# Optimization experiments

Measured on AMD Instinct MI355X. Metric: run time of the kernel, lower is better.

Reference implementation:

```python
import jax, jax.numpy as jnp
import numpy as np

B, LQ, D, DFF, NH, NL, NP = 16, 256, 256, 1024, 8, 4, 4
SHAPES = [(128, 128), (64, 64), (32, 32), (16, 16)]
S = sum(h * w for h, w in SHAPES)
DH = D // NH
OFFNORM = jnp.array([[w, h] for h, w in SHAPES], dtype=jnp.float32)  # (W,H) per level


def layer_norm(x, g, b, eps=1e-5):
    m = x.mean(-1, keepdims=True)
    v = jnp.mean((x - m) ** 2, axis=-1, keepdims=True)
    return (x - m) * jax.lax.rsqrt(v + eps) * g + b


def grid_sample_bilinear(img, grid):
    """img [N,C,H,W], grid [N,Hg,Wg,2] in [-1,1]; bilinear, zeros padding, align_corners=False."""
    N, C, H, W = img.shape
    Hg, Wg = grid.shape[1], grid.shape[2]
    x = (grid[..., 0] + 1.0) * (W * 0.5) - 0.5
    y = (grid[..., 1] + 1.0) * (H * 0.5) - 0.5
    x0 = jnp.floor(x); y0 = jnp.floor(y)
    wx1 = x - x0; wy1 = y - y0
    x0i = x0.astype(jnp.int32); y0i = y0.astype(jnp.int32)
    imgf = img.reshape(N, C, H * W)

    def tap(xi, yi, w):
        valid = (xi >= 0) & (xi < W) & (yi >= 0) & (yi < H)
        idx = (jnp.clip(yi, 0, H - 1) * W + jnp.clip(xi, 0, W - 1)).reshape(N, 1, Hg * Wg)
        return jnp.take_along_axis(imgf, idx, axis=2) * (w * valid).reshape(N, 1, Hg * Wg)

    out = (tap(x0i, y0i, (1 - wx1) * (1 - wy1)) + tap(x0i + 1, y0i, wx1 * (1 - wy1)) +
           tap(x0i, y0i + 1, (1 - wx1) * wy1) + tap(x0i + 1, y0i + 1, wx1 * wy1))
    return out.reshape(N, C, Hg, Wg)


def ms_sample(value, grids):
    """value [B,S,NH,DH], grids [B,Lq,NH,NL,NP,2] -> [B*NH, DH, Lq, NL*NP]."""
    Bv, Lq = value.shape[0], grids.shape[1]
    outs, start = [], 0
    for l, (h, w) in enumerate(SHAPES):
        v_l = value[:, start:start + h * w].transpose(0, 2, 3, 1).reshape(Bv * NH, DH, h, w)
        start += h * w
        g_l = grids[:, :, :, l].transpose(0, 2, 1, 3, 4).reshape(Bv * NH, Lq, NP, 2)
        outs.append(grid_sample_bilinear(v_l, g_l))  # [B*NH, DH, Lq, NP]
    return jnp.stack(outs, axis=3).reshape(Bv * NH, DH, Lq, NL * NP)


def mha(q, k, v, in_w, in_b, out_w, out_b, mask):
    d = q.shape[-1]
    Bq, Lq, Lk = q.shape[0], q.shape[1], k.shape[1]
    qh = (q @ in_w[:d].T + in_b[:d]).reshape(Bq, Lq, NH, DH).transpose(0, 2, 1, 3)
    kh = (k @ in_w[d:2 * d].T + in_b[d:2 * d]).reshape(Bq, Lk, NH, DH).transpose(0, 2, 1, 3)
    vh = (v @ in_w[2 * d:].T + in_b[2 * d:]).reshape(Bq, Lk, NH, DH).transpose(0, 2, 1, 3)
    logits = jnp.einsum('bhqd,bhkd->bhqk', qh, kh) * (DH ** -0.5) + mask
    o = jnp.einsum('bhqk,bhkd->bhqd', jax.nn.softmax(logits, axis=-1), vh)
    return o.transpose(0, 2, 1, 3).reshape(Bq, Lq, d) @ out_w.T + out_b


def _forward(tgt, query_pos, reference_points, src, tgt_masks,
             wq, wk, wv, so_w, so_b, sp_w, sp_b, aw_w, aw_b,
             sa_in_w, sa_in_b, sa_out_w, sa_out_b,
             ca_so_w, ca_so_b, ca_aw_w, ca_aw_b, ca_v_w, ca_v_b, ca_out_w, ca_out_b,
             l1_w, l1_b, l2_w, l2_b, n1_g, n1_b, n2_g, n2_b, n3_g, n3_b):
    # eval mode: dropout = identity; attn_concat_src=True; no kv cache.
    q = tgt @ wq.T + query_pos
    k = tgt @ wk.T
    v = tgt @ wv.T
    # ---- _sample_reference_points: grid_sample over levels, softmax over QUERY dim, sum over queries ----
    off = (tgt @ so_w.T + so_b).reshape(B, LQ, NH, NL, NP, 2)
    grids = 2.0 * (off / OFFNORM[None, None, None, :, None, :]) - 1.0
    aw = jax.nn.softmax((tgt @ aw_w.T + aw_b).reshape(B, LQ, NH, NL * NP), axis=1)
    value = (src @ sp_w.T + sp_b).reshape(B, S, NH, DH)
    sv = ms_sample(value, grids)                                       # [B*NH, DH, LQ, NL*NP]
    aw_r = aw.transpose(0, 2, 1, 3).reshape(B * NH, 1, LQ, NL * NP)
    sampled = (sv * aw_r).sum(axis=2).reshape(B, D, NL * NP).transpose(0, 2, 1)  # [B, NL*NP, D]
    # ---- self-attention with sampled src tokens prepended to k/v ----
    k = jnp.concatenate([sampled, k], axis=1)
    v = jnp.concatenate([sampled, v], axis=1)
    mask = jnp.concatenate([jnp.zeros((LQ, NL * NP), tgt.dtype), tgt_masks], axis=1)
    tgt = layer_norm(tgt + mha(q, k, v, sa_in_w, sa_in_b, sa_out_w, sa_out_b, mask), n2_g, n2_b)
    # ---- MSDeformAttn cross attention (2D reference points) ----
    qc = tgt + query_pos
    val2 = (src @ ca_v_w.T + ca_v_b).reshape(B, S, NH, DH)
    off2 = (qc @ ca_so_w.T + ca_so_b).reshape(B, LQ, NH, NL, NP, 2)
    aw2 = jax.nn.softmax((qc @ ca_aw_w.T + ca_aw_b).reshape(B, LQ, NH, NL * NP), axis=-1)
    loc2 = reference_points[:, :, None, :, None, :] + off2 / OFFNORM[None, None, None, :, None, :]
    sv2 = ms_sample(val2, 2.0 * loc2 - 1.0)                            # [B*NH, DH, LQ, NL*NP]
    out2 = (sv2 * aw2.transpose(0, 2, 1, 3).reshape(B * NH, 1, LQ, NL * NP)).sum(-1)
    out2 = out2.reshape(B, D, LQ).transpose(0, 2, 1) @ ca_out_w.T + ca_out_b
    tgt = layer_norm(tgt + out2, n1_g, n1_b)
    # ---- FFN ----
    ffn = jax.nn.relu(tgt @ l1_w.T + l1_b) @ l2_w.T + l2_b
    return layer_norm(tgt + ffn, n3_g, n3_b)


def setup_inputs():
    ks = iter(jax.random.split(jax.random.key(0), 48))
    rn = lambda s, sc=1.0: jax.random.normal(next(ks), s, dtype=jnp.float32) * sc
    W = 0.06  # ~1/sqrt(d_model)
    return dict(
        tgt=rn((B, LQ, D)),
        query_pos=rn((B, LQ, D)),
        reference_points=jax.random.uniform(next(ks), (B, LQ, NL, 2), dtype=jnp.float32),
        src=rn((B, S, D)),
        tgt_masks=jnp.zeros((LQ, LQ), jnp.float32),
        wq=rn((D, D), W), wk=rn((D, D), W), wv=rn((D, D), W),
        so_w=rn((NH * NL * NP * 2, D), 0.01),
        so_b=jax.random.uniform(next(ks), (NH * NL * NP * 2,), minval=-8.0, maxval=8.0),
        sp_w=rn((D, D), W), sp_b=rn((D,), W),
        aw_w=rn((NH * NL * NP, D), W), aw_b=rn((NH * NL * NP,), W),
        sa_in_w=rn((3 * D, D), W), sa_in_b=rn((3 * D,), W),
        sa_out_w=rn((D, D), W), sa_out_b=rn((D,), W),
        ca_so_w=rn((NH * NL * NP * 2, D), 0.01),
        ca_so_b=jax.random.uniform(next(ks), (NH * NL * NP * 2,), minval=-8.0, maxval=8.0),
        ca_aw_w=rn((NH * NL * NP, D), W), ca_aw_b=rn((NH * NL * NP,), W),
        ca_v_w=rn((D, D), W), ca_v_b=rn((D,), W),
        ca_out_w=rn((D, D), W), ca_out_b=rn((D,), W),
        l1_w=rn((DFF, D), W), l1_b=rn((DFF,), W),
        l2_w=rn((D, DFF), 0.03), l2_b=rn((D,), W),
        n1_g=jnp.ones((D,), jnp.float32), n1_b=jnp.zeros((D,), jnp.float32),
        n2_g=jnp.ones((D,), jnp.float32), n2_b=jnp.zeros((D,), jnp.float32),
        n3_g=jnp.ones((D,), jnp.float32), n3_b=jnp.zeros((D,), jnp.float32),
        src_spatial_shapes=jnp.array(SHAPES, jnp.int32),
        level_start_index=jnp.array(np.cumsum([0] + [h * w for h, w in SHAPES[:-1]]), jnp.int32),
    )


def reference(tgt, query_pos, reference_points, src, tgt_masks,
              wq, wk, wv, so_w, so_b, sp_w, sp_b, aw_w, aw_b,
              sa_in_w, sa_in_b, sa_out_w, sa_out_b,
              ca_so_w, ca_so_b, ca_aw_w, ca_aw_b, ca_v_w, ca_v_b, ca_out_w, ca_out_b,
              l1_w, l1_b, l2_w, l2_b, n1_g, n1_b, n2_g, n2_b, n3_g, n3_b,
              src_spatial_shapes, level_start_index):
    # src_spatial_shapes / level_start_index are static metadata (== SHAPES), baked in above.
    return _forward(tgt, query_pos, reference_points, src, tgt_masks,
                    wq, wk, wv, so_w, so_b, sp_w, sp_b, aw_w, aw_b,
                    sa_in_w, sa_in_b, sa_out_w, sa_out_b,
                    ca_so_w, ca_so_b, ca_aw_w, ca_aw_b, ca_v_w, ca_v_b, ca_out_w, ca_out_b,
                    l1_w, l1_b, l2_w, l2_b, n1_g, n1_b, n2_g, n2_b, n3_g, n3_b)
```

## Files before the change

### kernel.cpp

```cpp
#include <hip/hip_runtime.h>
#include <hip/hip_bf16.h>

#define NB   16
#define NLQ  256
#define ND   256
#define NDFF 1024
#define NNH  8
#define NNL  4
#define NNP  4
#define NDH  32
#define NS   21760
#define NLK  272

typedef __hip_bfloat16 bf16;
typedef unsigned short ushort_t;
typedef __bf16 bf16x8 __attribute__((ext_vector_type(8)));
typedef float f32x4 __attribute__((ext_vector_type(4)));
typedef unsigned short us4 __attribute__((ext_vector_type(4)));

__device__ __constant__ const int c_lvl_w[4]     = {128, 64, 32, 16};
__device__ __constant__ const int c_lvl_start[4] = {0, 16384, 20480, 21504};

__device__ __forceinline__ unsigned short f2bf(float x) {
  unsigned int u = __builtin_bit_cast(unsigned int, x);
  u += 0x7FFFu + ((u >> 16) & 1u);
  return (unsigned short)(u >> 16);
}

template<typename OT, bool RELU>
__global__ __launch_bounds__(256) void gemm_tn(const float* __restrict__ A,
                                               const float* __restrict__ W,
                                               const float* __restrict__ bias,
                                               const float* __restrict__ resid,
                                               OT* __restrict__ C,
                                               int M, int N, int K) {
  __shared__ float As[16][65];
  __shared__ float Ws[16][65];
  const int tid = threadIdx.x;
  const int tx = tid & 15, ty = tid >> 4;
  const int bn0 = blockIdx.x * 64, bm0 = blockIdx.y * 64;
  const int lr = tid >> 2;
  const int lk = (tid & 3) << 2;
  const float* Ap = A + (size_t)(bm0 + lr) * K + lk;
  const float* Wp = W + (size_t)(bn0 + lr) * K + lk;
  float acc[4][4] = {};
  for (int k0 = 0; k0 < K; k0 += 16) {
    float4 av = *(const float4*)(Ap + k0);
    float4 wv = *(const float4*)(Wp + k0);
    __syncthreads();
    As[lk + 0][lr] = av.x; As[lk + 1][lr] = av.y; As[lk + 2][lr] = av.z; As[lk + 3][lr] = av.w;
    Ws[lk + 0][lr] = wv.x; Ws[lk + 1][lr] = wv.y; Ws[lk + 2][lr] = wv.z; Ws[lk + 3][lr] = wv.w;
    __syncthreads();
#pragma unroll
    for (int k = 0; k < 16; ++k) {
      float a0 = As[k][ty * 4 + 0], a1 = As[k][ty * 4 + 1];
      float a2 = As[k][ty * 4 + 2], a3 = As[k][ty * 4 + 3];
      float b0 = Ws[k][tx * 4 + 0], b1 = Ws[k][tx * 4 + 1];
      float b2 = Ws[k][tx * 4 + 2], b3 = Ws[k][tx * 4 + 3];
      acc[0][0] += a0 * b0; acc[0][1] += a0 * b1; acc[0][2] += a0 * b2; acc[0][3] += a0 * b3;
      acc[1][0] += a1 * b0; acc[1][1] += a1 * b1; acc[1][2] += a1 * b2; acc[1][3] += a1 * b3;
      acc[2][0] += a2 * b0; acc[2][1] += a2 * b1; acc[2][2] += a2 * b2; acc[2][3] += a2 * b3;
      acc[3][0] += a3 * b0; acc[3][1] += a3 * b1; acc[3][2] += a3 * b2; acc[3][3] += a3 * b3;
    }
  }
#pragma unroll
  for (int i = 0; i < 4; ++i) {
    const int row = bm0 + ty * 4 + i;
#pragma unroll
    for (int j = 0; j < 4; ++j) {
      const int col = bn0 + tx * 4 + j;
      float c = acc[i][j];
      if (bias)  c += bias[col];
      if (resid) c += resid[(size_t)row * N + col];
      if (RELU)  c = fmaxf(c, 0.f);
      if constexpr (sizeof(OT) == 2) {
        C[(size_t)row * N + col] = __float2bfloat16(c);
      } else {
        C[(size_t)row * N + col] = c;
      }
    }
  }
}

__global__ __launch_bounds__(1024) void gemm_value_mfma(const float* __restrict__ A,
                                                        const ushort_t* __restrict__ Wb,
                                                        const float* __restrict__ bias,
                                                        ushort_t* __restrict__ C,
                                                        int M) {
  __shared__ __align__(16) ushort_t As[128][40];
  __shared__ __align__(16) ushort_t Bs[512][40];
  const int tid = threadIdx.x;
  const int wid = tid >> 6;
  const int lane = tid & 63;
  const int wm = wid >> 3;
  const int wn = wid & 7;
  const int bm0 = blockIdx.x * 128;
  const int lr = lane & 15;
  const int lk = (lane >> 4) * 8;

  const int ar = tid >> 3;
  const int ac4 = (tid & 7) * 4;
  const int br = tid >> 1;
  const int bc16 = (tid & 1) * 16;

  const float* Ap = A + (size_t)(bm0 + ar) * 256 + ac4;
  const ushort_t* Bp = Wb + (size_t)br * 256 + bc16;

  f32x4 acc[4][4] = {};

  for (int k0 = 0; k0 < 256; k0 += 32) {
    float4 av = *(const float4*)(Ap + k0);
    uint4 bv0 = *(const uint4*)(Bp + k0);
    uint4 bv1 = *(const uint4*)(Bp + k0 + 8);
    __syncthreads();
    us4 a4;
    a4[0] = f2bf(av.x); a4[1] = f2bf(av.y); a4[2] = f2bf(av.z); a4[3] = f2bf(av.w);
    *(us4*)&As[ar][ac4] = a4;
    *(uint4*)&Bs[br][bc16] = bv0;
    *(uint4*)&Bs[br][bc16 + 8] = bv1;
    __syncthreads();
    bf16x8 bfr[4];
#pragma unroll
    for (int ni = 0; ni < 4; ++ni)
      bfr[ni] = *(const bf16x8*)&Bs[wn * 64 + ni * 16 + lr][lk];
#pragma unroll
    for (int mi = 0; mi < 4; ++mi) {
      bf16x8 af = *(const bf16x8*)&As[wm * 64 + mi * 16 + lr][lk];
#pragma unroll
      for (int ni = 0; ni < 4; ++ni)
        acc[mi][ni] = __builtin_amdgcn_mfma_f32_16x16x32_bf16(af, bfr[ni], acc[mi][ni], 0, 0, 0);
    }
  }

  float bv[4];
#pragma unroll
  for (int ni = 0; ni < 4; ++ni) bv[ni] = bias[wn * 64 + ni * 16 + lr];
#pragma unroll
  for (int mi = 0; mi < 4; ++mi) {
#pragma unroll
    for (int r = 0; r < 4; ++r) {
      const int row = bm0 + wm * 64 + mi * 16 + (lane >> 4) * 4 + r;
#pragma unroll
      for (int ni = 0; ni < 4; ++ni) {
        const int col = wn * 64 + ni * 16 + lr;
        C[(size_t)row * 512 + col] = f2bf(acc[mi][ni][r] + bv[ni]);
      }
    }
  }
}

__global__ __launch_bounds__(256) void concat_w_kernel(const float* __restrict__ w1,
                                                       const float* __restrict__ w2,
                                                       const float* __restrict__ b1,
                                                       const float* __restrict__ b2,
                                                       ushort_t* __restrict__ wcat,
                                                       float* __restrict__ bcat) {
  int i = blockIdx.x * 256 + threadIdx.x;
  float v = (i < 65536) ? w1[i] : w2[i - 65536];
  wcat[i] = f2bf(v);
  if (i < 512) bcat[i] = (i < 256) ? b1[i] : b2[i - 256];
}

__global__ __launch_bounds__(64) void softmax_q_kernel(float* __restrict__ awl) {
  const int bc = blockIdx.x;
  const int c = bc & 127, b = bc >> 7;
  const int lane = threadIdx.x;
  float v[4];
  float mx = -1e30f;
#pragma unroll
  for (int i = 0; i < 4; ++i) {
    int q = lane + 64 * i;
    v[i] = awl[((size_t)(b * NLQ + q)) * 128 + c];
    mx = fmaxf(mx, v[i]);
  }
#pragma unroll
  for (int m = 32; m; m >>= 1) mx = fmaxf(mx, __shfl_xor(mx, m));
  float sum = 0.f;
#pragma unroll
  for (int i = 0; i < 4; ++i) { v[i] = __expf(v[i] - mx); sum += v[i]; }
#pragma unroll
  for (int m = 32; m; m >>= 1) sum += __shfl_xor(sum, m);
  float inv = 1.f / sum;
#pragma unroll
  for (int i = 0; i < 4; ++i) {
    int q = lane + 64 * i;
    awl[((size_t)(b * NLQ + q)) * 128 + c] = v[i] * inv;
  }
}

__global__ __launch_bounds__(128) void softmax16_kernel(float* __restrict__ aw2) {
  const int bq = blockIdx.x;
  const int c = threadIdx.x;
  float v = aw2[(size_t)bq * 128 + c];
  float mx = v;
#pragma unroll
  for (int m = 1; m < 16; m <<= 1) mx = fmaxf(mx, __shfl_xor(mx, m));
  float e = __expf(v - mx);
  float s = e;
#pragma unroll
  for (int m = 1; m < 16; m <<= 1) s += __shfl_xor(s, m);
  aw2[(size_t)bq * 128 + c] = e / s;
}

__global__ __launch_bounds__(256) void sample_sa_kernel(const bf16* __restrict__ vval,
                                                        const float* __restrict__ off1,
                                                        const float* __restrict__ aw,
                                                        float* __restrict__ sampled) {
  const int bid = blockIdx.x;
  const int lp = bid & 15, h = (bid >> 4) & 7, b = bid >> 7;
  const int l = lp >> 2, p = lp & 3;
  const int dh = threadIdx.x & 31, qg = threadIdx.x >> 5;
  const int Wd = c_lvl_w[l], st = c_lvl_start[l];
  const bf16* base = vval + ((size_t)b * NS + st) * 512 + h * 32 + dh;
  float acc = 0.f;
  for (int q = qg; q < NLQ; q += 8) {
    const float* op = off1 + (size_t)(b * NLQ + q) * 256 + ((h * 4 + l) * 4 + p) * 2;
    float x = op[0] - 0.5f;
    float y = op[1] - 0.5f;
    float w = aw[(size_t)(b * NLQ + q) * 128 + h * 16 + lp];
    float x0f = floorf(x), y0f = floorf(y);
    int x0 = (int)x0f, y0 = (int)y0f;
    float wx1 = x - x0f, wy1 = y - y0f;
    float wx0 = 1.f - wx1, wy0 = 1.f - wy1;
    auto tap = [&](int xi, int yi) -> float {
      if (xi < 0 || xi >= Wd || yi < 0 || yi >= Wd) return 0.f;
      return __bfloat162float(base[(size_t)(yi * Wd + xi) * 512]);
    };
    float v00 = tap(x0, y0),     v10 = tap(x0 + 1, y0);
    float v01 = tap(x0, y0 + 1), v11 = tap(x0 + 1, y0 + 1);
    acc += w * (wy0 * (wx0 * v00 + wx1 * v10) + wy1 * (wx0 * v01 + wx1 * v11));
  }
  __shared__ float red[8][32];
  red[qg][dh] = acc;
  __syncthreads();
  if (qg == 0) {
    float s = acc;
#pragma unroll
    for (int g = 1; g < 8; ++g) s += red[g][dh];
    sampled[((size_t)b * 16 + lp) * 256 + h * 32 + dh] = s;
  }
}

__global__ __launch_bounds__(256) void sample_ca_kernel(const bf16* __restrict__ vval,
                                                        const float* __restrict__ off2,
                                                        const float* __restrict__ aw2,
                                                        const float* __restrict__ refp,
                                                        float* __restrict__ out2) {
  const int bq = blockIdx.x;
  const int b = bq >> 8, q = bq & 255;
  const int h = threadIdx.x >> 5, dh = threadIdx.x & 31;
  float acc = 0.f;
#pragma unroll
  for (int lp = 0; lp < 16; ++lp) {
    const int l = lp >> 2, p = lp & 3;
    const int Wd = c_lvl_w[l], st = c_lvl_start[l];
    float rx = refp[((size_t)(b * NLQ + q) * 4 + l) * 2 + 0];
    float ry = refp[((size_t)(b * NLQ + q) * 4 + l) * 2 + 1];
    const float* op = off2 + (size_t)(b * NLQ + q) * 256 + ((h * 4 + l) * 4 + p) * 2;
    float x = rx * Wd + op[0] - 0.5f;
    float y = ry * Wd + op[1] - 0.5f;
    float w = aw2[(size_t)(b * NLQ + q) * 128 + h * 16 + lp];
    const bf16* base = vval + ((size_t)b * NS + st) * 512 + 256 + h * 32 + dh;
    float x0f = floorf(x), y0f = floorf(y);
    int x0 = (int)x0f, y0 = (int)y0f;
    float wx1 = x - x0f, wy1 = y - y0f;
    float wx0 = 1.f - wx1, wy0 = 1.f - wy1;
    auto tap = [&](int xi, int yi) -> float {
      if (xi < 0 || xi >= Wd || yi < 0 || yi >= Wd) return 0.f;
      return __bfloat162float(base[(size_t)(yi * Wd + xi) * 512]);
    };
    float v00 = tap(x0, y0),     v10 = tap(x0 + 1, y0);
    float v01 = tap(x0, y0 + 1), v11 = tap(x0 + 1, y0 + 1);
    acc += w * (wy0 * (wx0 * v00 + wx1 * v10) + wy1 * (wx0 * v01 + wx1 * v11));
  }
  out2[(size_t)(b * NLQ + q) * 256 + h * 32 + dh] = acc;
}

__global__ __launch_bounds__(256) void concat_kv_kernel(const float* __restrict__ sampled,
                                                        const float* __restrict__ kin,
                                                        const float* __restrict__ vin,
                                                        float* __restrict__ kcat,
                                                        float* __restrict__ vcat) {
  const int r = blockIdx.x;
  const int b = r / NLK, j = r % NLK;
  const int t = threadIdx.x;
  float kv, vv;
  if (j < 16) {
    kv = sampled[((size_t)b * 16 + j) * 256 + t];
    vv = kv;
  } else {
    kv = kin[((size_t)(b * NLQ + (j - 16))) * 256 + t];
    vv = vin[((size_t)(b * NLQ + (j - 16))) * 256 + t];
  }
  kcat[(size_t)r * 256 + t] = kv;
  vcat[(size_t)r * 256 + t] = vv;
}

__global__ __launch_bounds__(64) void attn_kernel(const float* __restrict__ qh,
                                                  const float* __restrict__ kh,
                                                  const float* __restrict__ vh,
                                                  const float* __restrict__ tmask,
                                                  float* __restrict__ attno) {
  const int bid = blockIdx.x;
  const int q = bid & 255, h = (bid >> 8) & 7, b = bid >> 11;
  const int lane = threadIdx.x;
  __shared__ float qrow[32];
  __shared__ float p[NLK];
  if (lane < 32) qrow[lane] = qh[((size_t)(b * NLQ + q)) * 256 + h * 32 + lane];
  __syncthreads();
  const float scale = 0.17677669529663687f;
  float s[5];
  float mx = -1e30f;
#pragma unroll
  for (int i = 0; i < 5; ++i) {
    int kk = lane + i * 64;
    float val = -1e30f;
    if (kk < NLK) {
      const float* kr = kh + ((size_t)(b * NLK + kk)) * 256 + h * 32;
      float d = 0.f;
#pragma unroll
      for (int c = 0; c < 32; ++c) d += qrow[c] * kr[c];
      val = d * scale;
      if (kk >= 16) val += tmask[(size_t)q * NLQ + (kk - 16)];
    }
    s[i] = val;
    mx = fmaxf(mx, val);
  }
#pragma unroll
  for (int m = 32; m; m >>= 1) mx = fmaxf(mx, __shfl_xor(mx, m));
  float sum = 0.f;
#pragma unroll
  for (int i = 0; i < 5; ++i) {
    int kk = lane + i * 64;
    if (kk < NLK) { s[i] = __expf(s[i] - mx); sum += s[i]; }
  }
#pragma unroll
  for (int m = 32; m; m >>= 1) sum += __shfl_xor(sum, m);
  const float inv = 1.f / sum;
#pragma unroll
  for (int i = 0; i < 5; ++i) {
    int kk = lane + i * 64;
    if (kk < NLK) p[kk] = s[i] * inv;
  }
  __syncthreads();
  if (lane < 32) {
    float acc = 0.f;
    const float* vb = vh + ((size_t)b * NLK) * 256 + h * 32 + lane;
    for (int kk = 0; kk < NLK; ++kk) acc += p[kk] * vb[(size_t)kk * 256];
    attno[((size_t)(b * NLQ + q)) * 256 + h * 32 + lane] = acc;
  }
}

__global__ __launch_bounds__(256) void add_ln_kernel(const float* __restrict__ resid,
                                                     const float* __restrict__ x,
                                                     const float* __restrict__ g,
                                                     const float* __restrict__ bt,
                                                     float* __restrict__ out) {
  const int row = blockIdx.x;
  const int t = threadIdx.x;
  const size_t idx = (size_t)row * 256 + t;
  float v = resid[idx] + x[idx];
  __shared__ float red[4];
  float s = v;
#pragma unroll
  for (int m = 32; m; m >>= 1) s += __shfl_xor(s, m);
  const int wid = t >> 6;
  if ((t & 63) == 0) red[wid] = s;
  __syncthreads();
  float mean = (red[0] + red[1] + red[2] + red[3]) * (1.f / 256.f);
  float d = v - mean;
  float s2 = d * d;
#pragma unroll
  for (int m = 32; m; m >>= 1) s2 += __shfl_xor(s2, m);
  __syncthreads();
  if ((t & 63) == 0) red[wid] = s2;
  __syncthreads();
  float var = (red[0] + red[1] + red[2] + red[3]) * (1.f / 256.f);
  out[idx] = d * rsqrtf(var + 1e-5f) * g[t] + bt[t];
}

__global__ __launch_bounds__(256) void add_kernel(const float* __restrict__ a,
                                                  const float* __restrict__ b,
                                                  float* __restrict__ c, int n) {
  int i = blockIdx.x * 256 + threadIdx.x;
  if (i < n) c[i] = a[i] + b[i];
}


static inline void gemm_f32(hipStream_t s, const float* A, const float* W,
                            const float* bias, const float* resid, float* C,
                            int M, int N, int K, bool relu = false) {
  dim3 g(N / 64, M / 64);
  if (relu) gemm_tn<float, true><<<g, 256, 0, s>>>(A, W, bias, resid, C, M, N, K);
  else      gemm_tn<float, false><<<g, 256, 0, s>>>(A, W, bias, resid, C, M, N, K);
}

extern "C" void kernel_launch(void* const* d_in, const int* in_sizes, int n_in,
                              void* d_out, int out_size, void* d_ws, size_t ws_size,
                              hipStream_t stream) {
  const float* tgt      = (const float*)d_in[0];
  const float* qpos     = (const float*)d_in[1];
  const float* refp     = (const float*)d_in[2];
  const float* src      = (const float*)d_in[3];
  const float* tmask    = (const float*)d_in[4];
  const float* wq       = (const float*)d_in[5];
  const float* wk       = (const float*)d_in[6];
  const float* wv       = (const float*)d_in[7];
  const float* so_w     = (const float*)d_in[8];
  const float* so_b     = (const float*)d_in[9];
  const float* sp_w     = (const float*)d_in[10];
  const float* sp_b     = (const float*)d_in[11];
  const float* aw_w     = (const float*)d_in[12];
  const float* aw_b     = (const float*)d_in[13];
  const float* sa_in_w  = (const float*)d_in[14];
  const float* sa_in_b  = (const float*)d_in[15];
  const float* sa_out_w = (const float*)d_in[16];
  const float* sa_out_b = (const float*)d_in[17];
  const float* ca_so_w  = (const float*)d_in[18];
  const float* ca_so_b  = (const float*)d_in[19];
  const float* ca_aw_w  = (const float*)d_in[20];
  const float* ca_aw_b  = (const float*)d_in[21];
  const float* ca_v_w   = (const float*)d_in[22];
  const float* ca_v_b   = (const float*)d_in[23];
  const float* ca_out_w = (const float*)d_in[24];
  const float* ca_out_b = (const float*)d_in[25];
  const float* l1_w     = (const float*)d_in[26];
  const float* l1_b     = (const float*)d_in[27];
  const float* l2_w     = (const float*)d_in[28];
  const float* l2_b     = (const float*)d_in[29];
  const float* n1_g     = (const float*)d_in[30];
  const float* n1_b     = (const float*)d_in[31];
  const float* n2_g     = (const float*)d_in[32];
  const float* n2_b     = (const float*)d_in[33];
  const float* n3_g     = (const float*)d_in[34];
  const float* n3_b     = (const float*)d_in[35];
  float* out = (float*)d_out;

  float* f = (float*)d_ws;
  size_t o = 0;
  auto alloc = [&](size_t n) { float* p = f + o; o += n; return p; };
  const size_t R = (size_t)NB * NLQ;
  const size_t RK = (size_t)NB * NLK;
  float* qb      = alloc(R * 256);
  float* kb      = alloc(R * 256);
  float* vb      = alloc(R * 256);
  float* off1    = alloc(R * 256);
  float* awl     = alloc(R * 128);
  float* sampled = alloc((size_t)NB * 16 * 256);
  float* kcat    = alloc(RK * 256);
  float* vcat    = alloc(RK * 256);
  float* qh      = alloc(R * 256);
  float* kh      = alloc(RK * 256);
  float* vh      = alloc(RK * 256);
  float* attno   = alloc(R * 256);
  float* attnp   = alloc(R * 256);
  float* tgt2    = alloc(R * 256);
  float* qc      = alloc(R * 256);
  float* off2    = alloc(R * 256);
  float* aw2     = alloc(R * 128);
  float* out2    = alloc(R * 256);
  float* out2p   = alloc(R * 256);
  float* tgt3    = alloc(R * 256);
  float* ffn1    = alloc(R * 1024);
  float* ffn2    = alloc(R * 256);
  ushort_t* wcat = (ushort_t*)alloc(512 * 256 / 2);
  float* bcat    = alloc(512);
  bf16* vval = (bf16*)(f + o);

  const int Msrc = NB * NS;

  concat_w_kernel<<<512, 256, 0, stream>>>(sp_w, ca_v_w, sp_b, ca_v_b, wcat, bcat);
  gemm_value_mfma<<<dim3(Msrc / 128), 1024, 0, stream>>>(src, wcat, bcat, (ushort_t*)vval, Msrc);

  gemm_f32(stream, tgt, wq,  nullptr, qpos, qb, (int)R, 256, 256);
  gemm_f32(stream, tgt, wk,  nullptr, nullptr, kb, (int)R, 256, 256);
  gemm_f32(stream, tgt, wv,  nullptr, nullptr, vb, (int)R, 256, 256);
  gemm_f32(stream, tgt, so_w, so_b,  nullptr, off1, (int)R, 256, 256);
  gemm_f32(stream, tgt, aw_w, aw_b,  nullptr, awl, (int)R, 128, 256);

  softmax_q_kernel<<<NB * 128, 64, 0, stream>>>(awl);
  sample_sa_kernel<<<NB * NNH * 16, 256, 0, stream>>>(vval, off1, awl, sampled);

  concat_kv_kernel<<<NB * NLK, 256, 0, stream>>>(sampled, kb, vb, kcat, vcat);
  gemm_f32(stream, qb,   sa_in_w,              sa_in_b,       nullptr, qh, (int)R, 256, 256);
  gemm_f32(stream, kcat, sa_in_w + 256 * 256,  sa_in_b + 256, nullptr, kh, (int)RK, 256, 256);
  gemm_f32(stream, vcat, sa_in_w + 512 * 256,  sa_in_b + 512, nullptr, vh, (int)RK, 256, 256);
  attn_kernel<<<NB * NNH * NLQ, 64, 0, stream>>>(qh, kh, vh, tmask, attno);
  gemm_f32(stream, attno, sa_out_w, sa_out_b, nullptr, attnp, (int)R, 256, 256);
  add_ln_kernel<<<(int)R, 256, 0, stream>>>(tgt, attnp, n2_g, n2_b, tgt2);

  add_kernel<<<(int)(R * 256 / 256), 256, 0, stream>>>(tgt2, qpos, qc, (int)(R * 256));
  gemm_f32(stream, qc, ca_so_w, ca_so_b, nullptr, off2, (int)R, 256, 256);
  gemm_f32(stream, qc, ca_aw_w, ca_aw_b, nullptr, aw2, (int)R, 128, 256);
  softmax16_kernel<<<(int)R, 128, 0, stream>>>(aw2);
  sample_ca_kernel<<<(int)R, 256, 0, stream>>>(vval, off2, aw2, refp, out2);
  gemm_f32(stream, out2, ca_out_w, ca_out_b, nullptr, out2p, (int)R, 256, 256);
  add_ln_kernel<<<(int)R, 256, 0, stream>>>(tgt2, out2p, n1_g, n1_b, tgt3);

  gemm_f32(stream, tgt3, l1_w, l1_b, nullptr, ffn1, (int)R, 1024, 256, true);
  gemm_f32(stream, ffn1, l2_w, l2_b, nullptr, ffn2, (int)R, 256, 1024);
  add_ln_kernel<<<(int)R, 256, 0, stream>>>(tgt3, ffn2, n3_g, n3_b, out);
}
```

Before: 1.591 ms.

## Replace fp32 SIMT GEMMs with bf16 MFMA GEMMs and merge projections sharing inputs

Every small fp32 GEMM now runs through a bf16 MFMA kernel, with all weights converted to bf16 once per call by a single prep kernel. The five tgt projections (q, k, v, offsets, attention weights) become one N=1152 GEMM, and the two cross-attention projections become one N=384 GEMM that adds qpos on the fly, which removes add_kernel. Downstream kernels read these packed outputs through new strides. The aim is to use the matrix cores and cut launch count, at the cost of bf16 rounding on activations and a weight conversion pass on every call.

```diff
diff --git a/kernel.cpp b/kernel.cpp
--- a/kernel.cpp
+++ b/kernel.cpp
@@ -27,56 +27,135 @@
   return (unsigned short)(u >> 16);
 }
 
-template<typename OT, bool RELU>
-__global__ __launch_bounds__(256) void gemm_tn(const float* __restrict__ A,
-                                               const float* __restrict__ W,
-                                               const float* __restrict__ bias,
-                                               const float* __restrict__ resid,
-                                               OT* __restrict__ C,
-                                               int M, int N, int K) {
-  __shared__ float As[16][65];
-  __shared__ float Ws[16][65];
+#define WOFF_V    0
+#define WOFF_TGT  131072
+#define WOFF_SA   425984
+#define WOFF_SAO  622592
+#define WOFF_CA   688128
+#define WOFF_CAO  786432
+#define WOFF_L1   851968
+#define WOFF_L2   1114112
+#define WTOT      1376256
+
+__global__ __launch_bounds__(256) void prep_kernel(
+    const float* __restrict__ sp_w, const float* __restrict__ ca_v_w,
+    const float* __restrict__ wq, const float* __restrict__ wk,
+    const float* __restrict__ wv, const float* __restrict__ so_w,
+    const float* __restrict__ aw_w, const float* __restrict__ sa_in_w,
+    const float* __restrict__ sa_out_w, const float* __restrict__ ca_so_w,
+    const float* __restrict__ ca_aw_w, const float* __restrict__ ca_out_w,
+    const float* __restrict__ l1_w, const float* __restrict__ l2_w,
+    const float* __restrict__ sp_b, const float* __restrict__ ca_v_b,
+    const float* __restrict__ so_b, const float* __restrict__ aw_b,
+    const float* __restrict__ ca_so_b, const float* __restrict__ ca_aw_b,
+    ushort_t* __restrict__ wout, float* __restrict__ bout) {
+  const int stride = gridDim.x * 256;
+  for (int i = blockIdx.x * 256 + threadIdx.x; i < WTOT + 2048; i += stride) {
+    if (i < WTOT) {
+      float v;
+      int j = i;
+      if (j < 131072) { v = (j < 65536) ? sp_w[j] : ca_v_w[j - 65536]; }
+      else if ((j -= 131072) < 294912) {
+        if      (j < 65536)  v = wq[j];
+        else if (j < 131072) v = wk[j - 65536];
+        else if (j < 196608) v = wv[j - 131072];
+        else if (j < 262144) v = so_w[j - 196608];
+        else                 v = aw_w[j - 262144];
+      }
+      else if ((j -= 294912) < 196608) v = sa_in_w[j];
+      else if ((j -= 196608) < 65536)  v = sa_out_w[j];
+      else if ((j -= 65536) < 98304)   v = (j < 65536) ? ca_so_w[j] : ca_aw_w[j - 65536];
+      else if ((j -= 98304) < 65536)   v = ca_out_w[j];
+      else if ((j -= 65536) < 262144)  v = l1_w[j];
+      else { j -= 262144; v = l2_w[j]; }
+      wout[i] = f2bf(v);
+    } else {
+      int j = i - WTOT;
+      float v;
+      if (j < 512) v = (j < 256) ? sp_b[j] : ca_v_b[j - 256];
+      else if (j < 1664) {
+        int t = j - 512;
+        v = (t < 768) ? 0.f : (t < 1024 ? so_b[t - 768] : aw_b[t - 1024]);
+      } else {
+        int t = j - 1664;
+        v = (t < 256) ? ca_so_b[t] : ca_aw_b[t - 256];
+      }
+      bout[j] = v;
+    }
+  }
+}
+
+template<bool RELU>
+__global__ __launch_bounds__(256) void gemm_bf16(const float* __restrict__ A,
+                                                 const float* __restrict__ A2,
+                                                 const ushort_t* __restrict__ Wb,
+                                                 const float* __restrict__ bias,
+                                                 const float* __restrict__ resid,
+                                                 float* __restrict__ C,
+                                                 int M, int N, int K,
+                                                 int lda, int ldc,
+                                                 int residN, int residLd) {
+  __shared__ __align__(16) ushort_t As[64][40];
+  __shared__ __align__(16) ushort_t Bs[64][40];
   const int tid = threadIdx.x;
-  const int tx = tid & 15, ty = tid >> 4;
+  const int wid = tid >> 6;
+  const int lane = tid & 63;
+  const int wr = wid >> 1, wc = wid & 1;
   const int bn0 = blockIdx.x * 64, bm0 = blockIdx.y * 64;
-  const int lr = tid >> 2;
-  const int lk = (tid & 3) << 2;
-  const float* Ap = A + (size_t)(bm0 + lr) * K + lk;
-  const float* Wp = W + (size_t)(bn0 + lr) * K + lk;
-  float acc[4][4] = {};
-  for (int k0 = 0; k0 < K; k0 += 16) {
-    float4 av = *(const float4*)(Ap + k0);
-    float4 wv = *(const float4*)(Wp + k0);
+  const int lr = lane & 15;
+  const int lk = (lane >> 4) * 8;
+
+  const int ar = tid >> 2;
+  const int ac8 = (tid & 3) * 8;
+  const float* Ap = A + (size_t)(bm0 + ar) * lda + ac8;
+  const float* A2p = A2 ? A2 + (size_t)(bm0 + ar) * lda + ac8 : nullptr;
+  const ushort_t* Wp = Wb + (size_t)(bn0 + ar) * K + ac8;
+
+  f32x4 acc[2][2] = {};
+
+  for (int k0 = 0; k0 < K; k0 += 32) {
+    float4 a0 = *(const float4*)(Ap + k0);
+    float4 a1 = *(const float4*)(Ap + k0 + 4);
+    uint4 bv = *(const uint4*)(Wp + k0);
+    if (A2p) {
+      float4 c0 = *(const float4*)(A2p + k0);
+      float4 c1 = *(const float4*)(A2p + k0 + 4);
+      a0.x += c0.x; a0.y += c0.y; a0.z += c0.z; a0.w += c0.w;
+      a1.x += c1.x; a1.y += c1.y; a1.z += c1.z; a1.w += c1.w;
+    }
     __syncthreads();
-    As[lk + 0][lr] = av.x; As[lk + 1][lr] = av.y; As[lk + 2][lr] = av.z; As[lk + 3][lr] = av.w;
-    Ws[lk + 0][lr] = wv.x; Ws[lk + 1][lr] = wv.y; Ws[lk + 2][lr] = wv.z; Ws[lk + 3][lr] = wv.w;
+    us4 lo, hi;
+    lo[0] = f2bf(a0.x); lo[1] = f2bf(a0.y); lo[2] = f2bf(a0.z); lo[3] = f2bf(a0.w);
+    hi[0] = f2bf(a1.x); hi[1] = f2bf(a1.y); hi[2] = f2bf(a1.z); hi[3] = f2bf(a1.w);
+    *(us4*)&As[ar][ac8] = lo;
+    *(us4*)&As[ar][ac8 + 4] = hi;
+    *(uint4*)&Bs[ar][ac8] = bv;
     __syncthreads();
-#pragma unroll
-    for (int k = 0; k < 16; ++k) {
-      float a0 = As[k][ty * 4 + 0], a1 = As[k][ty * 4 + 1];
-      float a2 = As[k][ty * 4 + 2], a3 = As[k][ty * 4 + 3];
-      float b0 = Ws[k][tx * 4 + 0], b1 = Ws[k][tx * 4 + 1];
-      float b2 = Ws[k][tx * 4 + 2], b3 = Ws[k][tx * 4 + 3];
-      acc[0][0] += a0 * b0; acc[0][1] += a0 * b1; acc[0][2] += a0 * b2; acc[0][3] += a0 * b3;
-      acc[1][0] += a1 * b0; acc[1][1] += a1 * b1; acc[1][2] += a1 * b2; acc[1][3] += a1 * b3;
-      acc[2][0] += a2 * b0; acc[2][1] += a2 * b1; acc[2][2] += a2 * b2; acc[2][3] += a2 * b3;
-      acc[3][0] += a3 * b0; acc[3][1] += a3 * b1; acc[3][2] += a3 * b2; acc[3][3] += a3 * b3;
-    }
-  }
-#pragma unroll
-  for (int i = 0; i < 4; ++i) {
-    const int row = bm0 + ty * 4 + i;
-#pragma unroll
-    for (int j = 0; j < 4; ++j) {
-      const int col = bn0 + tx * 4 + j;
-      float c = acc[i][j];
-      if (bias)  c += bias[col];
-      if (resid) c += resid[(size_t)row * N + col];
-      if (RELU)  c = fmaxf(c, 0.f);
-      if constexpr (sizeof(OT) == 2) {
-        C[(size_t)row * N + col] = __float2bfloat16(c);
-      } else {
-        C[(size_t)row * N + col] = c;
+    bf16x8 af[2], bf[2];
+#pragma unroll
+    for (int mi = 0; mi < 2; ++mi) af[mi] = *(const bf16x8*)&As[wr * 32 + mi * 16 + lr][lk];
+#pragma unroll
+    for (int ni = 0; ni < 2; ++ni) bf[ni] = *(const bf16x8*)&Bs[wc * 32 + ni * 16 + lr][lk];
+#pragma unroll
+    for (int mi = 0; mi < 2; ++mi)
+#pragma unroll
+      for (int ni = 0; ni < 2; ++ni)
+        acc[mi][ni] = __builtin_amdgcn_mfma_f32_16x16x32_bf16(af[mi], bf[ni], acc[mi][ni], 0, 0, 0);
+  }
+
+#pragma unroll
+  for (int mi = 0; mi < 2; ++mi) {
+#pragma unroll
+    for (int r = 0; r < 4; ++r) {
+      const int row = bm0 + wr * 32 + mi * 16 + (lane >> 4) * 4 + r;
+#pragma unroll
+      for (int ni = 0; ni < 2; ++ni) {
+        const int col = bn0 + wc * 32 + ni * 16 + lr;
+        float c = acc[mi][ni][r];
+        if (bias) c += bias[col];
+        if (resid && col < residN) c += resid[(size_t)row * residLd + col];
+        if (RELU) c = fmaxf(c, 0.f);
+        C[(size_t)row * ldc + col] = c;
       }
     }
   }
@@ -149,18 +228,6 @@
   }
 }
 
-__global__ __launch_bounds__(256) void concat_w_kernel(const float* __restrict__ w1,
-                                                       const float* __restrict__ w2,
-                                                       const float* __restrict__ b1,
-                                                       const float* __restrict__ b2,
-                                                       ushort_t* __restrict__ wcat,
-                                                       float* __restrict__ bcat) {
-  int i = blockIdx.x * 256 + threadIdx.x;
-  float v = (i < 65536) ? w1[i] : w2[i - 65536];
-  wcat[i] = f2bf(v);
-  if (i < 512) bcat[i] = (i < 256) ? b1[i] : b2[i - 256];
-}
-
 __global__ __launch_bounds__(64) void softmax_q_kernel(float* __restrict__ awl) {
   const int bc = blockIdx.x;
   const int c = bc & 127, b = bc >> 7;
@@ -170,7 +237,7 @@
 #pragma unroll
   for (int i = 0; i < 4; ++i) {
     int q = lane + 64 * i;
-    v[i] = awl[((size_t)(b * NLQ + q)) * 128 + c];
+    v[i] = awl[((size_t)(b * NLQ + q)) * 1152 + c];
     mx = fmaxf(mx, v[i]);
   }
 #pragma unroll
@@ -184,14 +251,14 @@
 #pragma unroll
   for (int i = 0; i < 4; ++i) {
     int q = lane + 64 * i;
-    awl[((size_t)(b * NLQ + q)) * 128 + c] = v[i] * inv;
+    awl[((size_t)(b * NLQ + q)) * 1152 + c] = v[i] * inv;
   }
 }
 
 __global__ __launch_bounds__(128) void softmax16_kernel(float* __restrict__ aw2) {
   const int bq = blockIdx.x;
   const int c = threadIdx.x;
-  float v = aw2[(size_t)bq * 128 + c];
+  float v = aw2[(size_t)bq * 384 + c];
   float mx = v;
 #pragma unroll
   for (int m = 1; m < 16; m <<= 1) mx = fmaxf(mx, __shfl_xor(mx, m));
@@ -199,7 +266,7 @@
   float s = e;
 #pragma unroll
   for (int m = 1; m < 16; m <<= 1) s += __shfl_xor(s, m);
-  aw2[(size_t)bq * 128 + c] = e / s;
+  aw2[(size_t)bq * 384 + c] = e / s;
 }
 
 __global__ __launch_bounds__(256) void sample_sa_kernel(const bf16* __restrict__ vval,
@@ -214,10 +281,10 @@
   const bf16* base = vval + ((size_t)b * NS + st) * 512 + h * 32 + dh;
   float acc = 0.f;
   for (int q = qg; q < NLQ; q += 8) {
-    const float* op = off1 + (size_t)(b * NLQ + q) * 256 + ((h * 4 + l) * 4 + p) * 2;
+    const float* op = off1 + (size_t)(b * NLQ + q) * 1152 + ((h * 4 + l) * 4 + p) * 2;
     float x = op[0] - 0.5f;
     float y = op[1] - 0.5f;
-    float w = aw[(size_t)(b * NLQ + q) * 128 + h * 16 + lp];
+    float w = aw[(size_t)(b * NLQ + q) * 1152 + h * 16 + lp];
     float x0f = floorf(x), y0f = floorf(y);
     int x0 = (int)x0f, y0 = (int)y0f;
     float wx1 = x - x0f, wy1 = y - y0f;
@@ -256,10 +323,10 @@
     const int Wd = c_lvl_w[l], st = c_lvl_start[l];
     float rx = refp[((size_t)(b * NLQ + q) * 4 + l) * 2 + 0];
     float ry = refp[((size_t)(b * NLQ + q) * 4 + l) * 2 + 1];
-    const float* op = off2 + (size_t)(b * NLQ + q) * 256 + ((h * 4 + l) * 4 + p) * 2;
+    const float* op = off2 + (size_t)(b * NLQ + q) * 384 + ((h * 4 + l) * 4 + p) * 2;
     float x = rx * Wd + op[0] - 0.5f;
     float y = ry * Wd + op[1] - 0.5f;
-    float w = aw2[(size_t)(b * NLQ + q) * 128 + h * 16 + lp];
+    float w = aw2[(size_t)(b * NLQ + q) * 384 + h * 16 + lp];
     const bf16* base = vval + ((size_t)b * NS + st) * 512 + 256 + h * 32 + dh;
     float x0f = floorf(x), y0f = floorf(y);
     int x0 = (int)x0f, y0 = (int)y0f;
@@ -289,8 +356,8 @@
     kv = sampled[((size_t)b * 16 + j) * 256 + t];
     vv = kv;
   } else {
-    kv = kin[((size_t)(b * NLQ + (j - 16))) * 256 + t];
-    vv = vin[((size_t)(b * NLQ + (j - 16))) * 256 + t];
+    kv = kin[((size_t)(b * NLQ + (j - 16))) * 1152 + t];
+    vv = vin[((size_t)(b * NLQ + (j - 16))) * 1152 + t];
   }
   kcat[(size_t)r * 256 + t] = kv;
   vcat[(size_t)r * 256 + t] = vv;
@@ -379,20 +446,14 @@
   out[idx] = d * rsqrtf(var + 1e-5f) * g[t] + bt[t];
 }
 
-__global__ __launch_bounds__(256) void add_kernel(const float* __restrict__ a,
-                                                  const float* __restrict__ b,
-                                                  float* __restrict__ c, int n) {
-  int i = blockIdx.x * 256 + threadIdx.x;
-  if (i < n) c[i] = a[i] + b[i];
-}
-
-
-static inline void gemm_f32(hipStream_t s, const float* A, const float* W,
-                            const float* bias, const float* resid, float* C,
-                            int M, int N, int K, bool relu = false) {
+
+static inline void gemm_b(hipStream_t s, const float* A, const float* A2,
+                          const ushort_t* Wb, const float* bias, const float* resid,
+                          float* C, int M, int N, int K, int lda, int ldc,
+                          int residN = 0, int residLd = 0, bool relu = false) {
   dim3 g(N / 64, M / 64);
-  if (relu) gemm_tn<float, true><<<g, 256, 0, s>>>(A, W, bias, resid, C, M, N, K);
-  else      gemm_tn<float, false><<<g, 256, 0, s>>>(A, W, bias, resid, C, M, N, K);
+  if (relu) gemm_bf16<true><<<g, 256, 0, s>>>(A, A2, Wb, bias, resid, C, M, N, K, lda, ldc, residN, residLd);
+  else      gemm_bf16<false><<<g, 256, 0, s>>>(A, A2, Wb, bias, resid, C, M, N, K, lda, ldc, residN, residLd);
 }
 
 extern "C" void kernel_launch(void* const* d_in, const int* in_sizes, int n_in,
@@ -441,11 +502,7 @@
   auto alloc = [&](size_t n) { float* p = f + o; o += n; return p; };
   const size_t R = (size_t)NB * NLQ;
   const size_t RK = (size_t)NB * NLK;
-  float* qb      = alloc(R * 256);
-  float* kb      = alloc(R * 256);
-  float* vb      = alloc(R * 256);
-  float* off1    = alloc(R * 256);
-  float* awl     = alloc(R * 128);
+  float* proj1   = alloc(R * 1152);
   float* sampled = alloc((size_t)NB * 16 * 256);
   float* kcat    = alloc(RK * 256);
   float* vcat    = alloc(RK * 256);
@@ -455,49 +512,57 @@
   float* attno   = alloc(R * 256);
   float* attnp   = alloc(R * 256);
   float* tgt2    = alloc(R * 256);
-  float* qc      = alloc(R * 256);
-  float* off2    = alloc(R * 256);
-  float* aw2     = alloc(R * 128);
+  float* proj2   = alloc(R * 384);
   float* out2    = alloc(R * 256);
   float* out2p   = alloc(R * 256);
   float* tgt3    = alloc(R * 256);
   float* ffn1    = alloc(R * 1024);
   float* ffn2    = alloc(R * 256);
-  ushort_t* wcat = (ushort_t*)alloc(512 * 256 / 2);
-  float* bcat    = alloc(512);
+  float* bprep   = alloc(2048);
+  ushort_t* wprep = (ushort_t*)alloc(WTOT / 2 + 64);
   bf16* vval = (bf16*)(f + o);
 
+  const float* qb_p   = proj1;
+  const float* kb_p   = proj1 + 256;
+  const float* vb_p   = proj1 + 512;
+  const float* off1_p = proj1 + 768;
+  float*       awl_p  = proj1 + 896;
+  float*       off2_p = proj2;
+  float*       aw2_p  = proj2 + 256;
+
   const int Msrc = NB * NS;
 
-  concat_w_kernel<<<512, 256, 0, stream>>>(sp_w, ca_v_w, sp_b, ca_v_b, wcat, bcat);
-  gemm_value_mfma<<<dim3(Msrc / 128), 1024, 0, stream>>>(src, wcat, bcat, (ushort_t*)vval, Msrc);
-
-  gemm_f32(stream, tgt, wq,  nullptr, qpos, qb, (int)R, 256, 256);
-  gemm_f32(stream, tgt, wk,  nullptr, nullptr, kb, (int)R, 256, 256);
-  gemm_f32(stream, tgt, wv,  nullptr, nullptr, vb, (int)R, 256, 256);
-  gemm_f32(stream, tgt, so_w, so_b,  nullptr, off1, (int)R, 256, 256);
-  gemm_f32(stream, tgt, aw_w, aw_b,  nullptr, awl, (int)R, 128, 256);
-
-  softmax_q_kernel<<<NB * 128, 64, 0, stream>>>(awl);
-  sample_sa_kernel<<<NB * NNH * 16, 256, 0, stream>>>(vval, off1, awl, sampled);
-
-  concat_kv_kernel<<<NB * NLK, 256, 0, stream>>>(sampled, kb, vb, kcat, vcat);
-  gemm_f32(stream, qb,   sa_in_w,              sa_in_b,       nullptr, qh, (int)R, 256, 256);
-  gemm_f32(stream, kcat, sa_in_w + 256 * 256,  sa_in_b + 256, nullptr, kh, (int)RK, 256, 256);
-  gemm_f32(stream, vcat, sa_in_w + 512 * 256,  sa_in_b + 512, nullptr, vh, (int)RK, 256, 256);
+  prep_kernel<<<2048, 256, 0, stream>>>(sp_w, ca_v_w, wq, wk, wv, so_w, aw_w,
+                                        sa_in_w, sa_out_w, ca_so_w, ca_aw_w,
+                                        ca_out_w, l1_w, l2_w,
+                                        sp_b, ca_v_b, so_b, aw_b, ca_so_b, ca_aw_b,
+                                        wprep, bprep);
+
+  gemm_value_mfma<<<dim3(Msrc / 128), 1024, 0, stream>>>(src, wprep + WOFF_V, bprep,
+                                                         (ushort_t*)vval, Msrc);
+
+  gemm_b(stream, tgt, nullptr, wprep + WOFF_TGT, bprep + 512, qpos,
+         proj1, (int)R, 1152, 256, 256, 1152, 256, 256);
+
+  softmax_q_kernel<<<NB * 128, 64, 0, stream>>>(awl_p);
+  sample_sa_kernel<<<NB * NNH * 16, 256, 0, stream>>>(vval, off1_p, awl_p, sampled);
+
+  concat_kv_kernel<<<NB * NLK, 256, 0, stream>>>(sampled, kb_p, vb_p, kcat, vcat);
+  gemm_b(stream, qb_p, nullptr, wprep + WOFF_SA,              sa_in_b,       nullptr, qh, (int)R, 256, 256, 1152, 256);
+  gemm_b(stream, kcat, nullptr, wprep + WOFF_SA + 256 * 256,  sa_in_b + 256, nullptr, kh, (int)RK, 256, 256, 256, 256);
+  gemm_b(stream, vcat, nullptr, wprep + WOFF_SA + 512 * 256,  sa_in_b + 512, nullptr, vh, (int)RK, 256, 256, 256, 256);
   attn_kernel<<<NB * NNH * NLQ, 64, 0, stream>>>(qh, kh, vh, tmask, attno);
-  gemm_f32(stream, attno, sa_out_w, sa_out_b, nullptr, attnp, (int)R, 256, 256);
+  gemm_b(stream, attno, nullptr, wprep + WOFF_SAO, sa_out_b, nullptr, attnp, (int)R, 256, 256, 256, 256);
   add_ln_kernel<<<(int)R, 256, 0, stream>>>(tgt, attnp, n2_g, n2_b, tgt2);
 
-  add_kernel<<<(int)(R * 256 / 256), 256, 0, stream>>>(tgt2, qpos, qc, (int)(R * 256));
-  gemm_f32(stream, qc, ca_so_w, ca_so_b, nullptr, off2, (int)R, 256, 256);
-  gemm_f32(stream, qc, ca_aw_w, ca_aw_b, nullptr, aw2, (int)R, 128, 256);
-  softmax16_kernel<<<(int)R, 128, 0, stream>>>(aw2);
-  sample_ca_kernel<<<(int)R, 256, 0, stream>>>(vval, off2, aw2, refp, out2);
-  gemm_f32(stream, out2, ca_out_w, ca_out_b, nullptr, out2p, (int)R, 256, 256);
+  gemm_b(stream, tgt2, qpos, wprep + WOFF_CA, bprep + 1664, nullptr,
+         proj2, (int)R, 384, 256, 256, 384);
+  softmax16_kernel<<<(int)R, 128, 0, stream>>>(aw2_p);
+  sample_ca_kernel<<<(int)R, 256, 0, stream>>>(vval, off2_p, aw2_p, refp, out2);
+  gemm_b(stream, out2, nullptr, wprep + WOFF_CAO, ca_out_b, nullptr, out2p, (int)R, 256, 256, 256, 256);
   add_ln_kernel<<<(int)R, 256, 0, stream>>>(tgt2, out2p, n1_g, n1_b, tgt3);
 
-  gemm_f32(stream, tgt3, l1_w, l1_b, nullptr, ffn1, (int)R, 1024, 256, true);
-  gemm_f32(stream, ffn1, l2_w, l2_b, nullptr, ffn2, (int)R, 256, 1024);
+  gemm_b(stream, tgt3, nullptr, wprep + WOFF_L1, l1_b, nullptr, ffn1, (int)R, 1024, 256, 256, 1024, 0, 0, true);
+  gemm_b(stream, ffn1, nullptr, wprep + WOFF_L2, l2_b, nullptr, ffn2, (int)R, 256, 1024, 1024, 256);
   add_ln_kernel<<<(int)R, 256, 0, stream>>>(tgt3, ffn2, n3_g, n3_b, out);
 }
```

New measurement: 1.291 ms. 18.9% less time.
